# Kernel tuning notes

Hardware: AMD Instinct MI355X
Metric: run time of the kernel (lower is better)

## Reference

```python
import jax, jax.numpy as jnp
import numpy as np

V, E, DIN, DH = 8192, 4096, 512, 256
N_CLASSES = 2
EPS = 1e-5  # torch LayerNorm default
EDGE_P = 0.004  # ~33 nodes per hyperedge


def layernorm(x, g, b):
    m = jnp.mean(x, axis=-1, keepdims=True)
    v = jnp.mean((x - m) ** 2, axis=-1, keepdims=True)
    return (x - m) / jnp.sqrt(v + EPS) * g + b


def setup_inputs() -> dict:
    key = jax.random.key(0)
    ks = jax.random.split(key, 8)
    X = jax.random.normal(ks[0], (V, DIN), dtype=jnp.float32)
    # binary incidence matrix (|V|, |E|)
    H_inc = (jax.random.uniform(ks[1], (V, E)) < EDGE_P).astype(jnp.float32)
    Wp = jax.random.normal(ks[2], (DH, DIN), dtype=jnp.float32) * 0.02  # input_proj (no bias)
    W0 = jax.random.normal(ks[3], (DH, DH), dtype=jnp.float32) * 0.02
    W1 = jax.random.normal(ks[4], (DH, DH), dtype=jnp.float32) * 0.02
    g0 = jnp.ones((DH,), jnp.float32); b0 = jnp.zeros((DH,), jnp.float32)
    g1 = jnp.ones((DH,), jnp.float32); b1 = jnp.zeros((DH,), jnp.float32)
    Wc = jax.random.normal(ks[5], (N_CLASSES, DH), dtype=jnp.float32) * 0.02
    bc = jnp.zeros((N_CLASSES,), jnp.float32)
    return {"X": X, "H_inc": H_inc, "Wp": Wp, "W0": W0, "W1": W1,
            "g0": g0, "b0": b0, "g1": g1, "b1": b1, "Wc": Wc, "bc": bc}


def reference(X, H_inc, Wp, W0, W1, g0, b0, g1, b1, Wc, bc):
    # --- normalized incidence: H_tilde = D_v^{-1/2} H D_e^{-1/2}, 0 for isolated ---
    d_v = H_inc.sum(axis=1)   # (V,)
    d_e = H_inc.sum(axis=0)   # (E,)
    dvi = jnp.where(d_v > 0, jnp.where(d_v > 0, d_v, 1.0) ** -0.5, 0.0)
    dei = jnp.where(d_e > 0, jnp.where(d_e > 0, d_e, 1.0) ** -0.5, 0.0)
    H_tilde = dvi[:, None] * H_inc * dei[None, :]            # (V, E)
    HHt = H_tilde @ H_tilde.T                                # (V, V)

    # input projection
    Xh = X @ Wp.T                                            # (V, DH)

    # L=2 message-passing layers with residual + LayerNorm
    for W, g, b in ((W0, g0, b0), (W1, g1, b1)):
        Xn = jax.nn.relu((HHt @ Xh) @ W.T)
        Xh = layernorm(Xh + Xn, g, b)

    # mean pool per hyperedge (== Python loop over E in the original):
    # z_e = mean of member node embeddings; zeros for empty hyperedges
    cnt = jnp.where(d_e > 0, d_e, 1.0)[:, None]              # (E, 1)
    z_E = (H_inc.T @ Xh) / cnt                               # (E, DH)

    logits = z_E @ Wc.T + bc                                 # (E, 2)
    return jax.nn.softmax(logits, axis=1)
```

## Files before the change

kernel.cpp:

```cpp
#include <hip/hip_runtime.h>
#include <math.h>

#define NV 8192
#define NE 4096
#define DIN 512
#define DH 256
#define CAP_E 96
#define CAP_V 64
#define NPROJ (NV / 32)
#define NSCAN (NV / 2)

#define OFF_XH   0
#define OFF_UB   (OFF_XH + NV*DH)
#define OFF_YB   (OFF_UB + NV*DH/2)
#define OFF_NCNT (OFF_YB + NE*DH/2)
#define OFF_ECNT (OFF_NCNT + NV)
#define OFF_EL   (OFF_ECNT + NE*16)
#define OFF_NL   (OFF_EL + NE*CAP_E)
#define OFF_XHB  (OFF_NL + NV*CAP_V)

using bf16x8 = __attribute__((ext_vector_type(8))) short;
using f32x4  = __attribute__((ext_vector_type(4))) float;
using f32x4v = __attribute__((ext_vector_type(4))) float;

__device__ inline unsigned short f2bf(float f) {
    union { float f; unsigned u; } v; v.f = f;
    unsigned r = v.u + 0x7FFF + ((v.u >> 16) & 1);
    return (unsigned short)(r >> 16);
}
__device__ inline float b2f(unsigned short s) {
    union { unsigned u; float f; } v; v.u = ((unsigned)s) << 16; return v.f;
}

__device__ inline void u_gemm_from_lds(const short* __restrict__ sm,
                                       const float* __restrict__ W,
                                       unsigned short* __restrict__ Ub,
                                       int bm, int tid) {
    const int w = tid >> 6, lane = tid & 63;
    const int r15 = lane & 15, k8 = (lane >> 4) << 3;
    const int swz = lane ^ ((lane >> 3) & 6);
    f32x4 acc[2][4];
#pragma unroll
    for (int mi = 0; mi < 2; ++mi)
#pragma unroll
        for (int ni = 0; ni < 4; ++ni) acc[mi][ni] = (f32x4){0.f, 0.f, 0.f, 0.f};
#pragma unroll
    for (int kc = 0; kc < 8; ++kc) {
        bf16x8 af[2], bfr[4];
        af[0] = *(const bf16x8*)&sm[(0 * 8 + kc) * 512 + swz * 8];
        af[1] = *(const bf16x8*)&sm[(1 * 8 + kc) * 512 + swz * 8];
#pragma unroll
        for (int ni = 0; ni < 4; ++ni) {
            const float* wr = W + (size_t)(w * 64 + ni * 16 + r15) * DH + kc * 32 + k8;
            float4 b0 = *(const float4*)wr;
            float4 b1 = *(const float4*)(wr + 4);
            bf16x8 bv;
            bv[0] = (short)f2bf(b0.x); bv[1] = (short)f2bf(b0.y);
            bv[2] = (short)f2bf(b0.z); bv[3] = (short)f2bf(b0.w);
            bv[4] = (short)f2bf(b1.x); bv[5] = (short)f2bf(b1.y);
            bv[6] = (short)f2bf(b1.z); bv[7] = (short)f2bf(b1.w);
            bfr[ni] = bv;
        }
#pragma unroll
        for (int mi = 0; mi < 2; ++mi)
#pragma unroll
            for (int ni = 0; ni < 4; ++ni)
                acc[mi][ni] = __builtin_amdgcn_mfma_f32_16x16x32_bf16(
                    af[mi], bfr[ni], acc[mi][ni], 0, 0, 0);
    }
    const int quad = lane >> 4, cl = lane & 15;
#pragma unroll
    for (int mi = 0; mi < 2; ++mi)
#pragma unroll
        for (int ni = 0; ni < 4; ++ni)
#pragma unroll
            for (int r = 0; r < 4; ++r)
                Ub[(size_t)(bm + mi * 16 + quad * 4 + r) * DH + w * 64 + ni * 16 + cl]
                    = f2bf(acc[mi][ni][r]);
}

__global__ __launch_bounds__(256) void scan_proj(const float* __restrict__ H,
                                                 const float* __restrict__ X,
                                                 const float* __restrict__ Wp,
                                                 const float* __restrict__ W0,
                                                 float* __restrict__ Xh,
                                                 unsigned short* __restrict__ Ub,
                                                 int* __restrict__ edge_cnt,
                                                 int* __restrict__ node_cnt,
                                                 int* __restrict__ edge_list,
                                                 int* __restrict__ node_list) {
    __shared__ short AsBs[1024 + 8192];
    const int tid = threadIdx.x;
    if (blockIdx.x >= NPROJ) {
        const int w = tid >> 6, lane = tid & 63;
        const int v    = (blockIdx.x - NPROJ) * 2 + (w >> 1);
        const int half = w & 1;
        const f32x4v* H4 = (const f32x4v*)(H + (size_t)v * NE) + half * 512;
        f32x4v h[8];
#pragma unroll
        for (int it = 0; it < 8; ++it)
            h[it] = __builtin_nontemporal_load(&H4[lane + 64 * it]);
        unsigned m = 0u;
#pragma unroll
        for (int it = 0; it < 8; ++it) {
#pragma unroll
            for (int c = 0; c < 4; ++c)
                m |= (h[it][c] != 0.0f ? 1u : 0u) << (it * 4 + c);
        }
        int n = __builtin_popcount(m);
        int pre = n;
#pragma unroll
        for (int o = 1; o < 64; o <<= 1) {
            int t = __shfl_up(pre, o, 64);
            if (lane >= o) pre += t;
        }
        int total = __shfl(pre, 63, 64);
        int local = pre - n;
        int base = 0;
        if (lane == 0 && total > 0) base = atomicAdd(&node_cnt[v], total);
        base = __shfl(base, 0, 64) + local;
        const int ebase = half * 2048 + 4 * lane;
        int e_arr[4] = {0, 0, 0, 0};
        {
            unsigned mm = m;
#pragma unroll
            for (int u = 0; u < 4; ++u) {
                if (mm) {
                    int j = __builtin_ctz(mm);
                    mm &= mm - 1;
                    e_arr[u] = ebase + 256 * (j >> 2) + (j & 3);
                }
            }
        }
        int s_arr[4];
#pragma unroll
        for (int u = 0; u < 4; ++u)
            s_arr[u] = (u < n) ? atomicAdd(&edge_cnt[e_arr[u] << 4], 1) : 0;
#pragma unroll
        for (int u = 0; u < 4; ++u) {
            if (u < n) {
                if (s_arr[u] < CAP_E) edge_list[e_arr[u] * CAP_E + s_arr[u]] = v;
                int idx = base + u;
                if (idx < CAP_V) node_list[v * CAP_V + idx] = e_arr[u];
            }
        }
        if (n > 4) {
            unsigned mm = m;
            mm &= mm - 1; mm &= mm - 1; mm &= mm - 1; mm &= mm - 1;
            int k = 4;
            while (mm) {
                int j = __builtin_ctz(mm); mm &= mm - 1;
                int ee = ebase + 256 * (j >> 2) + (j & 3);
                int gc = atomicAdd(&edge_cnt[ee << 4], 1);
                if (gc < CAP_E) edge_list[ee * CAP_E + gc] = v;
                int idx = base + k;
                if (idx < CAP_V) node_list[v * CAP_V + idx] = ee;
                ++k;
            }
        }
        return;
    }
    short* As = AsBs;
    short* Bs = AsBs + 1024;
    const int K = DIN;
    const int lane = tid & 63;
    const int w    = tid >> 6;
    const int bm   = blockIdx.x * 32;
    const int swz  = lane ^ ((lane >> 3) & 6);
    float4 ar, br[8];
    ar = *(const float4*)(X + (size_t)(bm + (tid >> 3)) * K + ((tid & 7) << 2));
#pragma unroll
    for (int it = 0; it < 8; ++it) {
        int i = tid + it * 256;
        br[it] = *(const float4*)(Wp + (size_t)(i >> 3) * K + ((i & 7) << 2));
    }
    f32x4 acc[2][4];
#pragma unroll
    for (int mi = 0; mi < 2; ++mi)
#pragma unroll
        for (int ni = 0; ni < 4; ++ni) acc[mi][ni] = (f32x4){0.f, 0.f, 0.f, 0.f};
    for (int k0 = 0; k0 < K; k0 += 32) {
        __syncthreads();
        {
            int row = tid >> 3, kk = (tid & 7) << 2;
            int quad = kk >> 3, j = kk & 7;
            int ln = (row & 15) + (quad << 4);
            int pp = ln ^ ((ln >> 3) & 6);
            ushort4 u = {f2bf(ar.x), f2bf(ar.y), f2bf(ar.z), f2bf(ar.w)};
            *(ushort4*)&As[(row >> 4) * 512 + pp * 8 + j] = u;
        }
#pragma unroll
        for (int it = 0; it < 8; ++it) {
            int i = tid + it * 256;
            int row = i >> 3, kk = (i & 7) << 2;
            int quad = kk >> 3, j = kk & 7;
            int ln = (row & 15) + (quad << 4);
            int pp = ln ^ ((ln >> 3) & 6);
            float4 v = br[it];
            ushort4 u = {f2bf(v.x), f2bf(v.y), f2bf(v.z), f2bf(v.w)};
            *(ushort4*)&Bs[(row >> 4) * 512 + pp * 8 + j] = u;
        }
        __syncthreads();
        if (k0 + 32 < K) {
            int kn = k0 + 32;
            ar = *(const float4*)(X + (size_t)(bm + (tid >> 3)) * K + kn + ((tid & 7) << 2));
#pragma unroll
            for (int it = 0; it < 8; ++it) {
                int i = tid + it * 256;
                br[it] = *(const float4*)(Wp + (size_t)(i >> 3) * K + kn + ((i & 7) << 2));
            }
        }
        bf16x8 af[2], bfr[4];
        af[0] = *(const bf16x8*)&As[0 * 512 + swz * 8];
        af[1] = *(const bf16x8*)&As[1 * 512 + swz * 8];
#pragma unroll
        for (int ni = 0; ni < 4; ++ni)
            bfr[ni] = *(const bf16x8*)&Bs[(w * 4 + ni) * 512 + swz * 8];
#pragma unroll
        for (int mi = 0; mi < 2; ++mi)
#pragma unroll
            for (int ni = 0; ni < 4; ++ni)
                acc[mi][ni] = __builtin_amdgcn_mfma_f32_16x16x32_bf16(
                    af[mi], bfr[ni], acc[mi][ni], 0, 0, 0);
    }
    const int quad = lane >> 4, cl = lane & 15;
    __syncthreads();
#pragma unroll
    for (int mi = 0; mi < 2; ++mi)
#pragma unroll
        for (int ni = 0; ni < 4; ++ni)
#pragma unroll
            for (int r = 0; r < 4; ++r) {
                float v = acc[mi][ni][r];
                int rl  = mi * 16 + quad * 4 + r;
                int col = w * 64 + ni * 16 + cl;
                Xh[(size_t)(bm + rl) * DH + col] = v;
                int kc = col >> 5, kk = col & 31;
                int q2 = kk >> 3, j = kk & 7;
                int ln = (rl & 15) + (q2 << 4);
                int pp = ln ^ ((ln >> 3) & 6);
                AsBs[(mi * 8 + kc) * 512 + pp * 8 + j] = (short)f2bf(v);
            }
    __syncthreads();
    u_gemm_from_lds(AsBs, W0, Ub, bm, tid);
}

__global__ __launch_bounds__(256) void gemm_u(const unsigned short* __restrict__ A,
                                              const float* __restrict__ W,
                                              unsigned short* __restrict__ U) {
    const int K = DH;
    __shared__ short As[2048];
    __shared__ short Bs[16384];
    const int tid  = threadIdx.x;
    const int lane = tid & 63;
    const int w    = tid >> 6;
    const int bm   = blockIdx.x * 32;
    const int swz  = lane ^ ((lane >> 3) & 6);

    uint4 ar; float4 br[16];
    ar = *(const uint4*)(A + (size_t)(bm + (tid >> 3)) * K + ((tid & 7) << 3));
#pragma unroll
    for (int it = 0; it < 16; ++it) {
        int i = tid + it * 256;
        br[it] = *(const float4*)(W + (size_t)(i >> 4) * K + ((i & 15) << 2));
    }
    f32x4 acc[2][4];
#pragma unroll
    for (int mi = 0; mi < 2; ++mi)
#pragma unroll
        for (int ni = 0; ni < 4; ++ni) acc[mi][ni] = (f32x4){0.f, 0.f, 0.f, 0.f};

    for (int k0 = 0; k0 < K; k0 += 64) {
        __syncthreads();
        {
            int row = tid >> 3, kq = tid & 7;
            int kc = kq >> 2, quad = kq & 3;
            int ln = (row & 15) + (quad << 4);
            int pp = ln ^ ((ln >> 3) & 6);
            *(uint4*)&As[((row >> 4) * 2 + kc) * 512 + pp * 8] = ar;
        }
#pragma unroll
        for (int it = 0; it < 16; ++it) {
            int i = tid + it * 256;
            int row = i >> 4, kk = (i & 15) << 2;
            int kc = kk >> 5, quad = (kk >> 3) & 3, j = kk & 7;
            int ln = (row & 15) + (quad << 4);
            int pp = ln ^ ((ln >> 3) & 6);
            float4 v = br[it];
            ushort4 u = {f2bf(v.x), f2bf(v.y), f2bf(v.z), f2bf(v.w)};
            *(ushort4*)&Bs[((row >> 4) * 2 + kc) * 512 + pp * 8 + j] = u;
        }
        __syncthreads();
        if (k0 + 64 < K) {
            int kn = k0 + 64;
            ar = *(const uint4*)(A + (size_t)(bm + (tid >> 3)) * K + kn + ((tid & 7) << 3));
#pragma unroll
            for (int it = 0; it < 16; ++it) {
                int i = tid + it * 256;
                br[it] = *(const float4*)(W + (size_t)(i >> 4) * K + kn + ((i & 15) << 2));
            }
        }
#pragma unroll
        for (int kc = 0; kc < 2; ++kc) {
            bf16x8 af[2], bfr[4];
            af[0] = *(const bf16x8*)&As[(0 * 2 + kc) * 512 + swz * 8];
            af[1] = *(const bf16x8*)&As[(1 * 2 + kc) * 512 + swz * 8];
#pragma unroll
            for (int ni = 0; ni < 4; ++ni)
                bfr[ni] = *(const bf16x8*)&Bs[((w * 4 + ni) * 2 + kc) * 512 + swz * 8];
#pragma unroll
            for (int mi = 0; mi < 2; ++mi)
#pragma unroll
                for (int ni = 0; ni < 4; ++ni)
                    acc[mi][ni] = __builtin_amdgcn_mfma_f32_16x16x32_bf16(
                        af[mi], bfr[ni], acc[mi][ni], 0, 0, 0);
        }
    }
    const int quad = lane >> 4, cl = lane & 15;
#pragma unroll
    for (int mi = 0; mi < 2; ++mi)
#pragma unroll
        for (int ni = 0; ni < 4; ++ni)
#pragma unroll
            for (int r = 0; r < 4; ++r)
                U[(size_t)(bm + mi * 16 + quad * 4 + r) * DH + w * 64 + ni * 16 + cl]
                    = f2bf(acc[mi][ni][r]);
}

__global__ __launch_bounds__(64) void edge_gather(const unsigned short* __restrict__ Ub,
                                                  const int* __restrict__ edge_cnt,
                                                  const int* __restrict__ edge_list,
                                                  const int* __restrict__ node_cnt,
                                                  unsigned short* __restrict__ Yb) {
    int e = blockIdx.x;
    int tid = threadIdx.x;
    __shared__ int   lv[CAP_E];
    __shared__ float lc[CAP_E];
    int tc = edge_cnt[e << 4];
    int cnt = min(tc, CAP_E);
    for (int j = tid; j < cnt; j += 64) {
        int v = edge_list[e * CAP_E + j];
        lv[j] = v * (DH / 4);
        lc[j] = rsqrtf((float)node_cnt[v]);
    }
    __syncthreads();
    const ushort4* X4 = (const ushort4*)Ub;
    float4 a[8];
#pragma unroll
    for (int u = 0; u < 8; ++u) a[u] = (float4){0.f, 0.f, 0.f, 0.f};
    int i = 0;
    for (; i + 8 <= cnt; i += 8) {
#pragma unroll
        for (int u = 0; u < 8; ++u) {
            ushort4 h = X4[lv[i + u] + tid]; float c = lc[i + u];
            a[u].x = fmaf(c, b2f(h.x), a[u].x); a[u].y = fmaf(c, b2f(h.y), a[u].y);
            a[u].z = fmaf(c, b2f(h.z), a[u].z); a[u].w = fmaf(c, b2f(h.w), a[u].w);
        }
    }
    for (; i < cnt; ++i) {
        ushort4 h = X4[lv[i] + tid]; float c = lc[i];
        a[0].x = fmaf(c, b2f(h.x), a[0].x); a[0].y = fmaf(c, b2f(h.y), a[0].y);
        a[0].z = fmaf(c, b2f(h.z), a[0].z); a[0].w = fmaf(c, b2f(h.w), a[0].w);
    }
#pragma unroll
    for (int u = 4; u > 0; u >>= 1)
#pragma unroll
        for (int q = 0; q < u; ++q) {
            a[q].x += a[q + u].x; a[q].y += a[q + u].y;
            a[q].z += a[q + u].z; a[q].w += a[q + u].w;
        }
    float de = tc > 0 ? rsqrtf((float)tc) : 0.f;
    ushort4 o = {f2bf(de * a[0].x), f2bf(de * a[0].y),
                 f2bf(de * a[0].z), f2bf(de * a[0].w)};
    ((ushort4*)Yb)[e * (DH / 4) + tid] = o;
}

__global__ __launch_bounds__(64) void node_ln(const unsigned short* __restrict__ Yb,
                                              const int* __restrict__ node_cnt,
                                              const int* __restrict__ node_list,
                                              const int* __restrict__ edge_cnt,
                                              float* __restrict__ Xh,
                                              unsigned short* __restrict__ Xhb,
                                              const float* __restrict__ g,
                                              const float* __restrict__ b) {
    int v = blockIdx.x;
    int tid = threadIdx.x;
    __shared__ int   le[CAP_V];
    __shared__ float lc[CAP_V];
    int tc = node_cnt[v];
    int cnt = min(tc, CAP_V);
    if (tid < cnt) {
        int e = node_list[v * CAP_V + tid];
        le[tid] = e * (DH / 4);
        lc[tid] = rsqrtf((float)edge_cnt[e << 4]);
    }
    __syncthreads();
    const ushort4* Y4 = (const ushort4*)Yb;
    float4 a[8];
#pragma unroll
    for (int u = 0; u < 8; ++u) a[u] = (float4){0.f, 0.f, 0.f, 0.f};
    int i = 0;
    for (; i + 8 <= cnt; i += 8) {
#pragma unroll
        for (int u = 0; u < 8; ++u) {
            ushort4 h = Y4[le[i + u] + tid]; float c = lc[i + u];
            a[u].x = fmaf(c, b2f(h.x), a[u].x); a[u].y = fmaf(c, b2f(h.y), a[u].y);
            a[u].z = fmaf(c, b2f(h.z), a[u].z); a[u].w = fmaf(c, b2f(h.w), a[u].w);
        }
    }
    for (; i < cnt; ++i) {
        ushort4 h = Y4[le[i] + tid]; float c = lc[i];
        a[0].x = fmaf(c, b2f(h.x), a[0].x); a[0].y = fmaf(c, b2f(h.y), a[0].y);
        a[0].z = fmaf(c, b2f(h.z), a[0].z); a[0].w = fmaf(c, b2f(h.w), a[0].w);
    }
#pragma unroll
    for (int u = 4; u > 0; u >>= 1)
#pragma unroll
        for (int q = 0; q < u; ++q) {
            a[q].x += a[q + u].x; a[q].y += a[q + u].y;
            a[q].z += a[q + u].z; a[q].w += a[q + u].w;
        }
    float dv = tc > 0 ? rsqrtf((float)tc) : 0.f;
    float4 xr = ((const float4*)Xh)[v * (DH / 4) + tid];
    float x0 = xr.x + fmaxf(dv * a[0].x, 0.f);
    float x1 = xr.y + fmaxf(dv * a[0].y, 0.f);
    float x2 = xr.z + fmaxf(dv * a[0].z, 0.f);
    float x3 = xr.w + fmaxf(dv * a[0].w, 0.f);
    float s = (x0 + x1) + (x2 + x3);
    float q = fmaf(x0, x0, fmaf(x1, x1, fmaf(x2, x2, x3 * x3)));
#pragma unroll
    for (int o = 1; o < 64; o <<= 1) {
        s += __shfl_xor(s, o, 64);
        q += __shfl_xor(q, o, 64);
    }
    float m = s * (1.0f / DH);
    float var = q * (1.0f / DH) - m * m;
    float rstd = rsqrtf(var + 1e-5f);
    float4 g4 = ((const float4*)g)[tid];
    float4 b4 = ((const float4*)b)[tid];
    float4 o;
    o.x = (x0 - m) * rstd * g4.x + b4.x;
    o.y = (x1 - m) * rstd * g4.y + b4.y;
    o.z = (x2 - m) * rstd * g4.z + b4.z;
    o.w = (x3 - m) * rstd * g4.w + b4.w;
    ((float4*)Xh)[v * (DH / 4) + tid] = o;
    ushort4 ob = {f2bf(o.x), f2bf(o.y), f2bf(o.z), f2bf(o.w)};
    ((ushort4*)Xhb)[v * (DH / 4) + tid] = ob;
}

__global__ __launch_bounds__(64) void pool_classify(const unsigned short* __restrict__ Xhb,
                                                    const int* __restrict__ edge_cnt,
                                                    const int* __restrict__ edge_list,
                                                    const float* __restrict__ Wc,
                                                    const float* __restrict__ bc,
                                                    float* __restrict__ out) {
    int e = blockIdx.x;
    int tid = threadIdx.x;
    __shared__ int lv[CAP_E];
    int tc = edge_cnt[e << 4];
    int cnt = min(tc, CAP_E);
    for (int j = tid; j < cnt; j += 64) lv[j] = edge_list[e * CAP_E + j] * (DH / 4);
    __syncthreads();
    const ushort4* X4 = (const ushort4*)Xhb;
    float4 a[8];
#pragma unroll
    for (int u = 0; u < 8; ++u) a[u] = (float4){0, 0, 0, 0};
    int i = 0;
    for (; i + 8 <= cnt; i += 8) {
#pragma unroll
        for (int u = 0; u < 8; ++u) {
            ushort4 h = X4[lv[i + u] + tid];
            a[u].x += b2f(h.x); a[u].y += b2f(h.y);
            a[u].z += b2f(h.z); a[u].w += b2f(h.w);
        }
    }
    for (; i < cnt; ++i) {
        ushort4 h = X4[lv[i] + tid];
        a[0].x += b2f(h.x); a[0].y += b2f(h.y);
        a[0].z += b2f(h.z); a[0].w += b2f(h.w);
    }
#pragma unroll
    for (int u = 4; u > 0; u >>= 1)
#pragma unroll
        for (int q = 0; q < u; ++q) {
            a[q].x += a[q + u].x; a[q].y += a[q + u].y;
            a[q].z += a[q + u].z; a[q].w += a[q + u].w;
        }
    float inv = tc > 0 ? 1.0f / (float)tc : 1.0f;
    float4 val = {a[0].x * inv, a[0].y * inv, a[0].z * inv, a[0].w * inv};
    const float4* W4 = (const float4*)Wc;
    float4 w0 = W4[tid], w1 = W4[64 + tid];
    float p0 = val.x * w0.x + val.y * w0.y + val.z * w0.z + val.w * w0.w;
    float p1 = val.x * w1.x + val.y * w1.y + val.z * w1.z + val.w * w1.w;
#pragma unroll
    for (int o = 32; o > 0; o >>= 1) {
        p0 += __shfl_down(p0, o, 64);
        p1 += __shfl_down(p1, o, 64);
    }
    if (tid == 0) {
        float l0 = p0 + bc[0], l1 = p1 + bc[1];
        float mx = fmaxf(l0, l1);
        float e0 = expf(l0 - mx), e1 = expf(l1 - mx);
        float s = 1.0f / (e0 + e1);
        out[e * 2 + 0] = e0 * s;
        out[e * 2 + 1] = e1 * s;
    }
}

extern "C" void kernel_launch(void* const* d_in, const int* in_sizes, int n_in,
                              void* d_out, int out_size, void* d_ws, size_t ws_size,
                              hipStream_t stream) {
    const float* X  = (const float*)d_in[0];
    const float* H  = (const float*)d_in[1];
    const float* Wp = (const float*)d_in[2];
    const float* W0 = (const float*)d_in[3];
    const float* W1 = (const float*)d_in[4];
    const float* g0 = (const float*)d_in[5];
    const float* b0 = (const float*)d_in[6];
    const float* g1 = (const float*)d_in[7];
    const float* b1 = (const float*)d_in[8];
    const float* Wc = (const float*)d_in[9];
    const float* bc = (const float*)d_in[10];
    float* out = (float*)d_out;

    float* ws = (float*)d_ws;
    float* Xh  = ws + OFF_XH;
    unsigned short* Ub  = (unsigned short*)(ws + OFF_UB);
    unsigned short* Yb  = (unsigned short*)(ws + OFF_YB);
    int* node_cnt  = (int*)(ws + OFF_NCNT);
    int* edge_cnt  = (int*)(ws + OFF_ECNT);
    int* edge_list = (int*)(ws + OFF_EL);
    int* node_list = (int*)(ws + OFF_NL);
    unsigned short* Xhb = (unsigned short*)(ws + OFF_XHB);

    hipMemsetAsync(node_cnt, 0, (size_t)(NV + NE * 16) * sizeof(int), stream);

    scan_proj<<<NPROJ + NSCAN, 256, 0, stream>>>(H, X, Wp, W0, Xh, Ub,
                                                 edge_cnt, node_cnt, edge_list, node_list);

    edge_gather<<<NE, 64, 0, stream>>>(Ub, edge_cnt, edge_list, node_cnt, Yb);
    node_ln<<<NV, 64, 0, stream>>>(Yb, node_cnt, node_list, edge_cnt,
                                   Xh, Xhb, g0, b0);
    gemm_u<<<NV / 32, 256, 0, stream>>>(Xhb, W1, Ub);
    edge_gather<<<NE, 64, 0, stream>>>(Ub, edge_cnt, edge_list, node_cnt, Yb);
    node_ln<<<NV, 64, 0, stream>>>(Yb, node_cnt, node_list, edge_cnt,
                                   Xh, Xhb, g1, b1);

    pool_classify<<<NE, 64, 0, stream>>>(Xhb, edge_cnt, edge_list, Wc, bc, out);
}
```

Measured before the change: 285.7 us.

## Project final node embeddings to class logits before hyperedge mean pooling

The classifier is linear, so each node's final LayerNorm output is projected onto the two class weights inside the last node LayerNorm kernel. The result is stored as a per-node float2 instead of the full bf16 embedding. Pooling then gathers only these two scalars per member node and averages them, which replaces the gather of full 256-wide embeddings per hyperedge. It adds a small workspace buffer. It also changes summation order, although the bf16 rounding of the embedding is kept.

```diff
diff --git a/kernel.cpp b/kernel.cpp
--- a/kernel.cpp
+++ b/kernel.cpp
@@ -18,6 +18,7 @@
 #define OFF_EL   (OFF_ECNT + NE*16)
 #define OFF_NL   (OFF_EL + NE*CAP_E)
 #define OFF_XHB  (OFF_NL + NV*CAP_V)
+#define OFF_Q    (OFF_XHB + NV*DH/2)
 
 using bf16x8 = __attribute__((ext_vector_type(8))) short;
 using f32x4  = __attribute__((ext_vector_type(4))) float;
@@ -448,36 +449,44 @@
     ((ushort4*)Xhb)[v * (DH / 4) + tid] = ob;
 }
 
-__global__ __launch_bounds__(64) void pool_classify(const unsigned short* __restrict__ Xhb,
-                                                    const int* __restrict__ edge_cnt,
-                                                    const int* __restrict__ edge_list,
-                                                    const float* __restrict__ Wc,
-                                                    const float* __restrict__ bc,
-                                                    float* __restrict__ out) {
-    int e = blockIdx.x;
+__global__ __launch_bounds__(64) void node_ln_q(const unsigned short* __restrict__ Yb,
+                                                const int* __restrict__ node_cnt,
+                                                const int* __restrict__ node_list,
+                                                const int* __restrict__ edge_cnt,
+                                                const float* __restrict__ Xh,
+                                                const float* __restrict__ g,
+                                                const float* __restrict__ b,
+                                                const float* __restrict__ Wc,
+                                                float2* __restrict__ qout) {
+    int v = blockIdx.x;
     int tid = threadIdx.x;
-    __shared__ int lv[CAP_E];
-    int tc = edge_cnt[e << 4];
-    int cnt = min(tc, CAP_E);
-    for (int j = tid; j < cnt; j += 64) lv[j] = edge_list[e * CAP_E + j] * (DH / 4);
+    __shared__ int   le[CAP_V];
+    __shared__ float lc[CAP_V];
+    int tc = node_cnt[v];
+    int cnt = min(tc, CAP_V);
+    if (tid < cnt) {
+        int e = node_list[v * CAP_V + tid];
+        le[tid] = e * (DH / 4);
+        lc[tid] = rsqrtf((float)edge_cnt[e << 4]);
+    }
     __syncthreads();
-    const ushort4* X4 = (const ushort4*)Xhb;
+    const ushort4* Y4 = (const ushort4*)Yb;
     float4 a[8];
 #pragma unroll
-    for (int u = 0; u < 8; ++u) a[u] = (float4){0, 0, 0, 0};
+    for (int u = 0; u < 8; ++u) a[u] = (float4){0.f, 0.f, 0.f, 0.f};
     int i = 0;
     for (; i + 8 <= cnt; i += 8) {
 #pragma unroll
         for (int u = 0; u < 8; ++u) {
-            ushort4 h = X4[lv[i + u] + tid];
-            a[u].x += b2f(h.x); a[u].y += b2f(h.y);
-            a[u].z += b2f(h.z); a[u].w += b2f(h.w);
+            ushort4 h = Y4[le[i + u] + tid]; float c = lc[i + u];
+            a[u].x = fmaf(c, b2f(h.x), a[u].x); a[u].y = fmaf(c, b2f(h.y), a[u].y);
+            a[u].z = fmaf(c, b2f(h.z), a[u].z); a[u].w = fmaf(c, b2f(h.w), a[u].w);
         }
     }
     for (; i < cnt; ++i) {
-        ushort4 h = X4[lv[i] + tid];
-        a[0].x += b2f(h.x); a[0].y += b2f(h.y);
-        a[0].z += b2f(h.z); a[0].w += b2f(h.w);
+        ushort4 h = Y4[le[i] + tid]; float c = lc[i];
+        a[0].x = fmaf(c, b2f(h.x), a[0].x); a[0].y = fmaf(c, b2f(h.y), a[0].y);
+        a[0].z = fmaf(c, b2f(h.z), a[0].z); a[0].w = fmaf(c, b2f(h.w), a[0].w);
     }
 #pragma unroll
     for (int u = 4; u > 0; u >>= 1)
@@ -486,24 +495,69 @@
             a[q].x += a[q + u].x; a[q].y += a[q + u].y;
             a[q].z += a[q + u].z; a[q].w += a[q + u].w;
         }
-    float inv = tc > 0 ? 1.0f / (float)tc : 1.0f;
-    float4 val = {a[0].x * inv, a[0].y * inv, a[0].z * inv, a[0].w * inv};
+    float dv = tc > 0 ? rsqrtf((float)tc) : 0.f;
+    float4 xr = ((const float4*)Xh)[v * (DH / 4) + tid];
+    float x0 = xr.x + fmaxf(dv * a[0].x, 0.f);
+    float x1 = xr.y + fmaxf(dv * a[0].y, 0.f);
+    float x2 = xr.z + fmaxf(dv * a[0].z, 0.f);
+    float x3 = xr.w + fmaxf(dv * a[0].w, 0.f);
+    float s = (x0 + x1) + (x2 + x3);
+    float q = fmaf(x0, x0, fmaf(x1, x1, fmaf(x2, x2, x3 * x3)));
+#pragma unroll
+    for (int o = 1; o < 64; o <<= 1) {
+        s += __shfl_xor(s, o, 64);
+        q += __shfl_xor(q, o, 64);
+    }
+    float m = s * (1.0f / DH);
+    float var = q * (1.0f / DH) - m * m;
+    float rstd = rsqrtf(var + 1e-5f);
+    float4 g4 = ((const float4*)g)[tid];
+    float4 b4 = ((const float4*)b)[tid];
+    float o0 = b2f(f2bf((x0 - m) * rstd * g4.x + b4.x));
+    float o1 = b2f(f2bf((x1 - m) * rstd * g4.y + b4.y));
+    float o2 = b2f(f2bf((x2 - m) * rstd * g4.z + b4.z));
+    float o3 = b2f(f2bf((x3 - m) * rstd * g4.w + b4.w));
     const float4* W4 = (const float4*)Wc;
     float4 w0 = W4[tid], w1 = W4[64 + tid];
-    float p0 = val.x * w0.x + val.y * w0.y + val.z * w0.z + val.w * w0.w;
-    float p1 = val.x * w1.x + val.y * w1.y + val.z * w1.z + val.w * w1.w;
+    float p0 = o0 * w0.x + o1 * w0.y + o2 * w0.z + o3 * w0.w;
+    float p1 = o0 * w1.x + o1 * w1.y + o2 * w1.z + o3 * w1.w;
+#pragma unroll
+    for (int off = 32; off > 0; off >>= 1) {
+        p0 += __shfl_down(p0, off, 64);
+        p1 += __shfl_down(p1, off, 64);
+    }
+    if (tid == 0) qout[v] = make_float2(p0, p1);
+}
+
+__global__ __launch_bounds__(256) void pool_q(const float2* __restrict__ q,
+                                              const int* __restrict__ edge_cnt,
+                                              const int* __restrict__ edge_list,
+                                              const float* __restrict__ bc,
+                                              float* __restrict__ out) {
+    const int tid = threadIdx.x;
+    const int w = tid >> 6, lane = tid & 63;
+    const int e = blockIdx.x * 4 + w;
+    int tc = edge_cnt[e << 4];
+    int cnt = min(tc, CAP_E);
+    float s0 = 0.f, s1 = 0.f;
+    for (int j = lane; j < cnt; j += 64) {
+        int v = edge_list[e * CAP_E + j];
+        float2 qq = q[v];
+        s0 += qq.x; s1 += qq.y;
+    }
 #pragma unroll
     for (int o = 32; o > 0; o >>= 1) {
-        p0 += __shfl_down(p0, o, 64);
-        p1 += __shfl_down(p1, o, 64);
-    }
-    if (tid == 0) {
-        float l0 = p0 + bc[0], l1 = p1 + bc[1];
+        s0 += __shfl_down(s0, o, 64);
+        s1 += __shfl_down(s1, o, 64);
+    }
+    if (lane == 0) {
+        float inv = tc > 0 ? 1.0f / (float)tc : 1.0f;
+        float l0 = s0 * inv + bc[0], l1 = s1 * inv + bc[1];
         float mx = fmaxf(l0, l1);
         float e0 = expf(l0 - mx), e1 = expf(l1 - mx);
-        float s = 1.0f / (e0 + e1);
-        out[e * 2 + 0] = e0 * s;
-        out[e * 2 + 1] = e1 * s;
+        float sden = 1.0f / (e0 + e1);
+        out[e * 2 + 0] = e0 * sden;
+        out[e * 2 + 1] = e1 * sden;
     }
 }
 
@@ -532,6 +586,7 @@
     int* edge_list = (int*)(ws + OFF_EL);
     int* node_list = (int*)(ws + OFF_NL);
     unsigned short* Xhb = (unsigned short*)(ws + OFF_XHB);
+    float2* qbuf = (float2*)(ws + OFF_Q);
 
     hipMemsetAsync(node_cnt, 0, (size_t)(NV + NE * 16) * sizeof(int), stream);
 
@@ -543,8 +598,8 @@
                                    Xh, Xhb, g0, b0);
     gemm_u<<<NV / 32, 256, 0, stream>>>(Xhb, W1, Ub);
     edge_gather<<<NE, 64, 0, stream>>>(Ub, edge_cnt, edge_list, node_cnt, Yb);
-    node_ln<<<NV, 64, 0, stream>>>(Yb, node_cnt, node_list, edge_cnt,
-                                   Xh, Xhb, g1, b1);
-
-    pool_classify<<<NE, 64, 0, stream>>>(Xhb, edge_cnt, edge_list, Wc, bc, out);
-}
+    node_ln_q<<<NV, 64, 0, stream>>>(Yb, node_cnt, node_list, edge_cnt,
+                                     Xh, g1, b1, Wc, qbuf);
+
+    pool_q<<<NE / 4, 256, 0, stream>>>(qbuf, edge_cnt, edge_list, bc, out);
+}
```

Measured after the change: 281.2 us. Within noise of the previous version (-1.6%).
